# Kernel optimization log

Hardware: AMD Instinct MI355X
Metric: run time of the kernel (lower is better)

The kernel has to match this reference:

```python
import jax, jax.numpy as jnp
import numpy as np

N = 512          # nsites (even)
B = 1024         # batch of spin configurations
HALF = N // 2

# static off-diagonal scatter indices (~eye mask)
_ROWS, _COLS = np.nonzero(~np.eye(N, dtype=bool))


def setup_inputs() -> dict:
    key = jax.random.key(0)
    k_f, k_x = jax.random.split(key)
    scale = np.float32(np.sqrt(2.0 * np.e / N))
    F = jax.random.normal(k_f, (N * N - N,), jnp.float32) * scale
    # balanced +/-1 spins per sample (zero magnetization), random permutation per row
    base = jnp.concatenate([jnp.ones(HALF, jnp.float32), -jnp.ones(HALF, jnp.float32)])
    keys = jax.random.split(k_x, B)
    x = jax.vmap(lambda k: jax.random.permutation(k, base))(keys)
    return {"x": x, "F": F}


def reference(x, F):
    # scatter parameters into dense off-diagonal pair matrix (shared across batch)
    F_full = jnp.zeros((N, N), F.dtype).at[_ROWS, _COLS].set(F)

    def single(xs):
        # spin system: up occupation then down occupation -> exactly N particles
        occ = jnp.concatenate([xs > 0, xs <= 0])
        idx = jnp.flatnonzero(occ, size=N)          # [N] int
        up = idx[:HALF]                              # up-site indices in [0, N)
        dn = idx[HALF:] - N                          # down-site indices in [0, N)
        sub = F_full[up[:, None], dn[None, :]]       # [N/2, N/2] gathered submatrix
        return jnp.linalg.det(sub)

    return jax.vmap(single)(x)  # [B]
```

## Files before the change

kernel.cpp:

```cpp
#include <hip/hip_runtime.h>

#define NN 512
#define NM1 511
#define PCT(r, j) pcT[(r) * 13 + (j)]

#define T16(X, K) X(K,0) X(K,1) X(K,2) X(K,3) X(K,4) X(K,5) X(K,6) X(K,7) \
  X(K,8) X(K,9) X(K,10) X(K,11) X(K,12) X(K,13) X(K,14) X(K,15)
#define T4x16(X) T16(X,0) T16(X,1) T16(X,2) T16(X,3)
#define T16S(X) X(0) X(1) X(2) X(3) X(4) X(5) X(6) X(7) \
  X(8) X(9) X(10) X(11) X(12) X(13) X(14) X(15)
#define P8(X, K) X(K,0) X(K,1) X(K,2) X(K,3) X(K,4) X(K,5) X(K,6) X(K,7)
#define P4x8(X) P8(X,0) P8(X,1) P8(X,2) P8(X,3)

__device__ __forceinline__ float rdlane(float v, int l) {
  return __uint_as_float(
      (unsigned)__builtin_amdgcn_readlane((int)__float_as_uint(v), l));
}
__device__ __forceinline__ float fastrcp(float v) {
  float r;
  asm("v_rcp_f32 %0, %1" : "=v"(r) : "v"(v));
  return r;
}

__global__ __attribute__((amdgpu_waves_per_eu(4, 4))) __launch_bounds__(1024)
void det_lu_kernel(
    const float* __restrict__ x,
    const float* __restrict__ F,
    float* __restrict__ out) {
  __shared__ __align__(16) float pcT[256 * 13];
  __shared__ __align__(16) float lbuf[8 * 256];
  __shared__ __align__(16) float Ubuf[8 * 260];
  __shared__ float livef[256];
  __shared__ int   perm[256];
  __shared__ int   upbuf[256];
  __shared__ int   dnbuf[256];
  __shared__ int   wavecnt[8];
  __shared__ int   totinv;
  __shared__ float ldspad[12100];

  const int tid = threadIdx.x;
  const int L   = tid & 63;
  const int w   = tid >> 6;

  const float* xrow = x + (size_t)blockIdx.x * NN;

  if ((int)blockIdx.x < 0) ((volatile float*)ldspad)[tid] = 1.0f;

  bool pos = false;
  unsigned long long mask = 0;
  if (tid < NN) {
    float xv = xrow[tid];
    pos = xv > 0.0f;
    mask = __ballot(pos);
    if (L == 0) wavecnt[w] = __popcll(mask);
  }
  if (tid == 0) totinv = 0;
  if (tid < 256) livef[tid] = 1.0f;
  __syncthreads();
  if (tid < NN) {
    int base = 0;
    for (int i = 0; i < w; i++) base += wavecnt[i];
    int pbelow = __popcll(mask & ((1ull << L) - 1ull));
    if (pos) upbuf[base + pbelow] = tid;
    else     dnbuf[(64 * w - base) + (L - pbelow)] = tid;
  }
  __syncthreads();

#define DECLC(M) const int cg##M = dnbuf[16 * w + (M)];
  T16S(DECLC)
  const int rg0 = upbuf[L];
  const int rg1 = upbuf[L + 64];
  const int rg2 = upbuf[L + 128];
  const int rg3 = upbuf[L + 192];
#define DECLA(K, M)                                                         \
  float a##K##_##M = (cg##M == rg##K)                                       \
      ? 0.0f                                                                \
      : F[(size_t)rg##K * NM1 + cg##M - (cg##M > rg##K ? 1 : 0)];
  T4x16(DECLA)

  if (w == 0) {
#define S0(K, M) if ((M) < 8) PCT(L + 64 * (K), (M)) = a##K##_##M;
    T4x16(S0)
  }
  double det = 1.0;
  __syncthreads();

#define DPPMAX(CTRL) {                                                      \
    unsigned _t = (unsigned)__builtin_amdgcn_update_dpp(                    \
        0, (int)key, (CTRL), 0xf, 0xf, false);                              \
    key = key > _t ? key : _t; }
#define BCJ(K, J, S) if ((J) >= (S)) uv##J = rdlane(pr##K##_##J, lp);
#define BCARM(K, S)                                                         \
    if (kp == (K)) { BCJ(K,0,S) BCJ(K,1,S) BCJ(K,2,S) BCJ(K,3,S)            \
                     BCJ(K,4,S) BCJ(K,5,S) BCJ(K,6,S) BCJ(K,7,S) }
#define LSTEP(K, S)                                                         \
    float l##K = ((dead4 >> (K)) & 1u) ? 0.0f : pr##K##_##S * invp;         \
    pr##K##_##S = l##K;
#define UPD(K, J, S)                                                        \
    if ((J) > (S)) pr##K##_##J = fmaf(-l##K, uv##J, pr##K##_##J);
#define UPDJ(J, S) UPD(0,J,S) UPD(1,J,S) UPD(2,J,S) UPD(3,J,S)
#define FSTEP(S) {                                                          \
    unsigned b0 = (dead4 & 1u) ? 0u                                         \
        : ((__float_as_uint(fabsf(pr0_##S)) & 0xFFFFFF00u) | (unsigned)L);  \
    unsigned b1 = (dead4 & 2u) ? 0u                                         \
        : ((__float_as_uint(fabsf(pr1_##S)) & 0xFFFFFF00u) | (unsigned)(L + 64)); \
    unsigned b2 = (dead4 & 4u) ? 0u                                         \
        : ((__float_as_uint(fabsf(pr2_##S)) & 0xFFFFFF00u) | (unsigned)(L + 128)); \
    unsigned b3 = (dead4 & 8u) ? 0u                                         \
        : ((__float_as_uint(fabsf(pr3_##S)) & 0xFFFFFF00u) | (unsigned)(L + 192)); \
    unsigned m01 = b0 > b1 ? b0 : b1, m23 = b2 > b3 ? b2 : b3;              \
    unsigned key = m01 > m23 ? m01 : m23;                                   \
    DPPMAX(0x111) DPPMAX(0x112) DPPMAX(0x114) DPPMAX(0x118)                 \
    DPPMAX(0x142) DPPMAX(0x143)                                             \
    const int pv = __builtin_amdgcn_readlane((int)key, 63) & 255;           \
    const int kp = pv >> 6, lp = pv & 63;                                   \
    if (lp == L) dead4 |= 1u << kp;                                         \
    float uv0 = 0.f, uv1 = 0.f, uv2 = 0.f, uv3 = 0.f;                       \
    float uv4 = 0.f, uv5 = 0.f, uv6 = 0.f, uv7 = 0.f;                       \
    BCARM(0,S) BCARM(1,S) BCARM(2,S) BCARM(3,S)                             \
    const float piv = uv##S;                                                \
    det *= (double)piv;                                                     \
    const float invp = fastrcp(piv);                                        \
    LSTEP(0,S) LSTEP(1,S) LSTEP(2,S) LSTEP(3,S)                             \
    UPDJ(0,S) UPDJ(1,S) UPDJ(2,S) UPDJ(3,S)                                 \
    UPDJ(4,S) UPDJ(5,S) UPDJ(6,S) UPDJ(7,S)                                 \
    lbuf[(S) * 256 + L      ] = l0;                                         \
    lbuf[(S) * 256 + L +  64] = l1;                                         \
    lbuf[(S) * 256 + L + 128] = l2;                                         \
    lbuf[(S) * 256 + L + 192] = l3;                                         \
    if (L == lp) livef[pv] = 0.0f;                                          \
    if (L == 0) perm[P * 8 + (S)] = pv;                                     \
  }

#define STQW(T, K)                                                          \
    if (L == (p##T & 63)) {                                                 \
      const int ub = (T) * 260 + 16 * w;                                    \
      *reinterpret_cast<float4*>(&Ubuf[ub + 0]) =                           \
          make_float4(a##K##_0, a##K##_1, a##K##_2, a##K##_3);              \
      *reinterpret_cast<float4*>(&Ubuf[ub + 4]) =                           \
          make_float4(a##K##_4, a##K##_5, a##K##_6, a##K##_7);              \
      *reinterpret_cast<float4*>(&Ubuf[ub + 8]) =                           \
          make_float4(a##K##_8, a##K##_9, a##K##_10, a##K##_11);            \
      *reinterpret_cast<float4*>(&Ubuf[ub + 12]) =                          \
          make_float4(a##K##_12, a##K##_13, a##K##_14, a##K##_15);          \
    }
#define STASHT(T) {                                                         \
    const int kpt = p##T >> 6;                                              \
    if (kpt == 0)      { STQW(T, 0) }                                       \
    else if (kpt == 1) { STQW(T, 1) }                                       \
    else if (kpt == 2) { STQW(T, 2) }                                       \
    else               { STQW(T, 3) }                                       \
  }

#define TUROW(K, A, B, C, D)                                                \
    a##K##_##A = fmaf(-lk##K, uq.x, a##K##_##A);                            \
    a##K##_##B = fmaf(-lk##K, uq.y, a##K##_##B);                            \
    a##K##_##C = fmaf(-lk##K, uq.z, a##K##_##C);                            \
    a##K##_##D = fmaf(-lk##K, uq.w, a##K##_##D);
#define TUQ(A, B, C, D)                                                     \
    TUROW(0, A, B, C, D) TUROW(1, A, B, C, D)                               \
    TUROW(2, A, B, C, D) TUROW(3, A, B, C, D)

#pragma unroll 1
  for (int P = 0; P < 32; P++) {
    const bool trailing = (2 * w + 1 > P);

    if (w == 0) {
#define LDP(K, J) float pr##K##_##J = PCT(L + 64 * (K), (J));
      P4x8(LDP)
      unsigned dead4 = 0u;
      FSTEP(0) FSTEP(1) FSTEP(2) FSTEP(3)
      FSTEP(4) FSTEP(5) FSTEP(6) FSTEP(7)
    }
    __syncthreads();

    if (trailing) {
      const int p0 = perm[P * 8 + 0], p1 = perm[P * 8 + 1];
      const int p2 = perm[P * 8 + 2], p3 = perm[P * 8 + 3];
      const int p4 = perm[P * 8 + 4], p5 = perm[P * 8 + 5];
      const int p6 = perm[P * 8 + 6], p7 = perm[P * 8 + 7];
      STASHT(0) STASHT(1) STASHT(2) STASHT(3)
      STASHT(4) STASHT(5) STASHT(6) STASHT(7)
      asm volatile("s_waitcnt lgkmcnt(0)" ::: "memory");

      if (L < 16) {
        const int jb = 16 * w + L;
        float u[8];
#pragma unroll
        for (int t = 0; t < 8; t++) {
          const int pt = perm[P * 8 + t];
          float acc = Ubuf[t * 260 + jb];
#pragma unroll
          for (int s2 = 0; s2 < t; s2++)
            acc = fmaf(-lbuf[s2 * 256 + pt], u[s2], acc);
          u[t] = acc;
          Ubuf[t * 260 + jb] = acc;
        }
      }
      asm volatile("s_waitcnt lgkmcnt(0)" ::: "memory");

#pragma unroll 1
      for (int t = 0; t < 8; t++) {
        const int lb = t * 256 + L;
        const float lk0 = lbuf[lb];
        const float lk1 = lbuf[lb + 64];
        const float lk2 = lbuf[lb + 128];
        const float lk3 = lbuf[lb + 192];
        const float* ub = &Ubuf[t * 260 + 16 * w];
        { const float4 uq = *reinterpret_cast<const float4*>(ub + 0);
          TUQ(0, 1, 2, 3) }
        { const float4 uq = *reinterpret_cast<const float4*>(ub + 4);
          TUQ(4, 5, 6, 7) }
        { const float4 uq = *reinterpret_cast<const float4*>(ub + 8);
          TUQ(8, 9, 10, 11) }
        { const float4 uq = *reinterpret_cast<const float4*>(ub + 12);
          TUQ(12, 13, 14, 15) }
      }
    }
    {
      const int wstar = (P + 1) >> 1, h = (P + 1) & 1;
      if (P < 31 && w == wstar) {
        const float lv0 = livef[L];
        const float lv1 = livef[L + 64];
        const float lv2 = livef[L + 128];
        const float lv3 = livef[L + 192];
#define SEa(K, M) if ((M) < 8)  PCT(L + 64*(K), (M))     = a##K##_##M * lv##K;
#define SEb(K, M) if ((M) >= 8) PCT(L + 64*(K), (M) - 8) = a##K##_##M * lv##K;
        if (h == 0) { T4x16(SEa) }
        else        { T4x16(SEb) }
      }
    }
    __syncthreads();
  }

  int myinv = 0;
  {
    const int i0 = tid & 255;
    const int cbase = (tid >> 8) * 64;
    const int pi = perm[i0];
#pragma unroll 8
    for (int j = 0; j < 64; j++) {
      int jj = cbase + j;
      if (jj > i0 && perm[jj] < pi) myinv++;
    }
  }
#pragma unroll
  for (int off = 32; off; off >>= 1) myinv += __shfl_xor(myinv, off);
  if (L == 0) atomicAdd(&totinv, myinv);
  __syncthreads();
  if (tid == 0) out[blockIdx.x] = (float)((totinv & 1) ? -det : det);
}

extern "C" void kernel_launch(void* const* d_in, const int* in_sizes, int n_in,
                              void* d_out, int out_size, void* d_ws, size_t ws_size,
                              hipStream_t stream) {
  const float* x = (const float*)d_in[0];
  const float* F = (const float*)d_in[1];
  float* out = (float*)d_out;
  const int B = out_size;
  hipLaunchKernelGGL(det_lu_kernel, dim3(B), dim3(1024), 0, stream, x, F, out);
}
```

Before: 980.4 us.

## Double-buffer L/U panels and defer trailing update to overlap next panel factorization

Double-buffers the L and U panel buffers so most waves apply the trailing rank-8 update from the previous panel while wave 0 factorizes the current panel. Only the wave that owns the next panel applies its update immediately, before staging the next pivot columns. This moves trailing-update work off the critical path between barriers. In exchange it uses more LDS (the padding is shrunk to keep occupancy) and adds an unroll-2 update loop that raises register pressure.

```diff
diff --git a/kernel.cpp b/kernel.cpp
--- a/kernel.cpp
+++ b/kernel.cpp
@@ -28,15 +28,15 @@
     const float* __restrict__ F,
     float* __restrict__ out) {
   __shared__ __align__(16) float pcT[256 * 13];
-  __shared__ __align__(16) float lbuf[8 * 256];
-  __shared__ __align__(16) float Ubuf[8 * 260];
+  __shared__ __align__(16) float lbufD[2][8 * 256];
+  __shared__ __align__(16) float UbufD[2][8 * 260];
   __shared__ float livef[256];
   __shared__ int   perm[256];
   __shared__ int   upbuf[256];
   __shared__ int   dnbuf[256];
   __shared__ int   wavecnt[8];
   __shared__ int   totinv;
-  __shared__ float ldspad[12100];
+  __shared__ float ldspad[7900];
 
   const int tid = threadIdx.x;
   const int L   = tid & 63;
@@ -124,24 +124,24 @@
     LSTEP(0,S) LSTEP(1,S) LSTEP(2,S) LSTEP(3,S)                             \
     UPDJ(0,S) UPDJ(1,S) UPDJ(2,S) UPDJ(3,S)                                 \
     UPDJ(4,S) UPDJ(5,S) UPDJ(6,S) UPDJ(7,S)                                 \
-    lbuf[(S) * 256 + L      ] = l0;                                         \
-    lbuf[(S) * 256 + L +  64] = l1;                                         \
-    lbuf[(S) * 256 + L + 128] = l2;                                         \
-    lbuf[(S) * 256 + L + 192] = l3;                                         \
+    lbP[(S) * 256 + L      ] = l0;                                          \
+    lbP[(S) * 256 + L +  64] = l1;                                          \
+    lbP[(S) * 256 + L + 128] = l2;                                          \
+    lbP[(S) * 256 + L + 192] = l3;                                          \
     if (L == lp) livef[pv] = 0.0f;                                          \
     if (L == 0) perm[P * 8 + (S)] = pv;                                     \
   }
 
 #define STQW(T, K)                                                          \
     if (L == (p##T & 63)) {                                                 \
-      const int ub = (T) * 260 + 16 * w;                                    \
-      *reinterpret_cast<float4*>(&Ubuf[ub + 0]) =                           \
+      float* ubw = &ubP[(T) * 260 + 16 * w];                                \
+      *reinterpret_cast<float4*>(ubw + 0) =                                 \
           make_float4(a##K##_0, a##K##_1, a##K##_2, a##K##_3);              \
-      *reinterpret_cast<float4*>(&Ubuf[ub + 4]) =                           \
+      *reinterpret_cast<float4*>(ubw + 4) =                                 \
           make_float4(a##K##_4, a##K##_5, a##K##_6, a##K##_7);              \
-      *reinterpret_cast<float4*>(&Ubuf[ub + 8]) =                           \
+      *reinterpret_cast<float4*>(ubw + 8) =                                 \
           make_float4(a##K##_8, a##K##_9, a##K##_10, a##K##_11);            \
-      *reinterpret_cast<float4*>(&Ubuf[ub + 12]) =                          \
+      *reinterpret_cast<float4*>(ubw + 12) =                                \
           make_float4(a##K##_12, a##K##_13, a##K##_14, a##K##_15);          \
     }
 #define STASHT(T) {                                                         \
@@ -160,10 +160,34 @@
 #define TUQ(A, B, C, D)                                                     \
     TUROW(0, A, B, C, D) TUROW(1, A, B, C, D)                               \
     TUROW(2, A, B, C, D) TUROW(3, A, B, C, D)
+#define TUTLOOP(LB_, UB_)                                                   \
+    _Pragma("unroll 2")                                                     \
+    for (int t = 0; t < 8; t++) {                                           \
+      const float lk0 = (LB_)[t * 256 + L];                                 \
+      const float lk1 = (LB_)[t * 256 + L + 64];                            \
+      const float lk2 = (LB_)[t * 256 + L + 128];                           \
+      const float lk3 = (LB_)[t * 256 + L + 192];                           \
+      const float* ub_ = &(UB_)[t * 260 + 16 * w];                          \
+      { const float4 uq = *reinterpret_cast<const float4*>(ub_ + 0);        \
+        TUQ(0, 1, 2, 3) }                                                   \
+      { const float4 uq = *reinterpret_cast<const float4*>(ub_ + 4);        \
+        TUQ(4, 5, 6, 7) }                                                   \
+      { const float4 uq = *reinterpret_cast<const float4*>(ub_ + 8);        \
+        TUQ(8, 9, 10, 11) }                                                 \
+      { const float4 uq = *reinterpret_cast<const float4*>(ub_ + 12);       \
+        TUQ(12, 13, 14, 15) }                                               \
+    }
 
 #pragma unroll 1
   for (int P = 0; P < 32; P++) {
-    const bool trailing = (2 * w + 1 > P);
+    const int bsel = P & 1;
+    float* const lbP = lbufD[bsel];
+    float* const ubP = UbufD[bsel];
+    const float* const lbQ = lbufD[bsel ^ 1];
+    const float* const ubQ = UbufD[bsel ^ 1];
+    const bool trailingP = (2 * w + 1 > P);
+    const bool trailPrev =
+        (P > 0) && (2 * w + 1 > P - 1) && (w != (P >> 1));
 
     if (w == 0) {
 #define LDP(K, J) float pr##K##_##J = PCT(L + 64 * (K), (J));
@@ -171,10 +195,12 @@
       unsigned dead4 = 0u;
       FSTEP(0) FSTEP(1) FSTEP(2) FSTEP(3)
       FSTEP(4) FSTEP(5) FSTEP(6) FSTEP(7)
+    } else if (trailPrev) {
+      TUTLOOP(lbQ, ubQ)
     }
     __syncthreads();
 
-    if (trailing) {
+    if (trailingP) {
       const int p0 = perm[P * 8 + 0], p1 = perm[P * 8 + 1];
       const int p2 = perm[P * 8 + 2], p3 = perm[P * 8 + 3];
       const int p4 = perm[P * 8 + 4], p5 = perm[P * 8 + 5];
@@ -182,44 +208,26 @@
       STASHT(0) STASHT(1) STASHT(2) STASHT(3)
       STASHT(4) STASHT(5) STASHT(6) STASHT(7)
       asm volatile("s_waitcnt lgkmcnt(0)" ::: "memory");
-
       if (L < 16) {
         const int jb = 16 * w + L;
         float u[8];
 #pragma unroll
         for (int t = 0; t < 8; t++) {
           const int pt = perm[P * 8 + t];
-          float acc = Ubuf[t * 260 + jb];
+          float acc = ubP[t * 260 + jb];
 #pragma unroll
           for (int s2 = 0; s2 < t; s2++)
-            acc = fmaf(-lbuf[s2 * 256 + pt], u[s2], acc);
+            acc = fmaf(-lbP[s2 * 256 + pt], u[s2], acc);
           u[t] = acc;
-          Ubuf[t * 260 + jb] = acc;
+          ubP[t * 260 + jb] = acc;
         }
       }
       asm volatile("s_waitcnt lgkmcnt(0)" ::: "memory");
-
-#pragma unroll 1
-      for (int t = 0; t < 8; t++) {
-        const int lb = t * 256 + L;
-        const float lk0 = lbuf[lb];
-        const float lk1 = lbuf[lb + 64];
-        const float lk2 = lbuf[lb + 128];
-        const float lk3 = lbuf[lb + 192];
-        const float* ub = &Ubuf[t * 260 + 16 * w];
-        { const float4 uq = *reinterpret_cast<const float4*>(ub + 0);
-          TUQ(0, 1, 2, 3) }
-        { const float4 uq = *reinterpret_cast<const float4*>(ub + 4);
-          TUQ(4, 5, 6, 7) }
-        { const float4 uq = *reinterpret_cast<const float4*>(ub + 8);
-          TUQ(8, 9, 10, 11) }
-        { const float4 uq = *reinterpret_cast<const float4*>(ub + 12);
-          TUQ(12, 13, 14, 15) }
-      }
     }
     {
       const int wstar = (P + 1) >> 1, h = (P + 1) & 1;
       if (P < 31 && w == wstar) {
+        TUTLOOP(lbP, ubP)
         const float lv0 = livef[L];
         const float lv1 = livef[L + 64];
         const float lv2 = livef[L + 128];
```

Measured after the change: 921.8 us. -6.0%, faster.
